# Optimization experiments

Hardware: AMD Instinct MI355X
Metric: run time of the kernel (lower is better)

The kernel has to match this reference:

```python
import jax, jax.numpy as jnp
import numpy as np

EMBED = 128
HEADS = 16
N = 10000
E = 160000
NEG_SLOPE = 0.2


def setup_inputs() -> dict:
    key = jax.random.key(0)
    ks = jax.random.split(key, 12)
    s = 0.05
    return {
        "x": jax.random.normal(ks[0], (N, EMBED), jnp.float32),
        "edge_index": jax.random.randint(ks[1], (2, E), 0, N, jnp.int64),
        # gat1: in=EMBED, out=EMBED, heads=16, concat
        "W1": jax.random.normal(ks[2], (EMBED, HEADS * EMBED), jnp.float32) * s,
        "a_src1": jax.random.normal(ks[3], (HEADS, EMBED), jnp.float32) * s,
        "a_dst1": jax.random.normal(ks[4], (HEADS, EMBED), jnp.float32) * s,
        "b1": jnp.zeros((HEADS * EMBED,), jnp.float32),
        # gat2: in=HEADS*EMBED, out=EMBED, heads=1, no concat
        "W2": jax.random.normal(ks[5], (HEADS * EMBED, EMBED), jnp.float32) * s,
        "a_src2": jax.random.normal(ks[6], (1, EMBED), jnp.float32) * s,
        "a_dst2": jax.random.normal(ks[7], (1, EMBED), jnp.float32) * s,
        "b2": jnp.zeros((EMBED,), jnp.float32),
        # classifier
        "Wc": jax.random.normal(ks[8], (EMBED, 1), jnp.float32) * s,
        "bc": jnp.zeros((1,), jnp.float32),
    }


def _gat_layer(x, src, dst, W, a_src, a_dst, b, heads, out_ch, n_nodes):
    # node projection: [N, H, C]
    h = (x @ W).reshape(n_nodes, heads, out_ch)
    # per-node attention logits [N, H]
    al_s = jnp.einsum('nhc,hc->nh', h, a_src)
    al_d = jnp.einsum('nhc,hc->nh', h, a_dst)
    # per-edge logits [E, H]
    e = jax.nn.leaky_relu(al_s[src] + al_d[dst], NEG_SLOPE)
    # segment softmax over incoming edges of each dst node
    m = jax.ops.segment_max(e, dst, num_segments=n_nodes)
    ex = jnp.exp(e - m[dst])
    z = jax.ops.segment_sum(ex, dst, num_segments=n_nodes)
    alpha = ex / (z[dst] + 1e-16)
    # weighted scatter-aggregate [N, H, C]
    msg = h[src] * alpha[:, :, None]
    out = jax.ops.segment_sum(msg, dst, num_segments=n_nodes)
    return out.reshape(n_nodes, heads * out_ch) + b


def reference(x, edge_index, W1, a_src1, a_dst1, b1, W2, a_src2, a_dst2, b2, Wc, bc):
    n_nodes = x.shape[0]
    # PyG GATConv default: add self loops
    loop = jnp.arange(n_nodes, dtype=edge_index.dtype)
    src = jnp.concatenate([edge_index[0], loop])
    dst = jnp.concatenate([edge_index[1], loop])
    h = _gat_layer(x, src, dst, W1, a_src1, a_dst1, b1, HEADS, EMBED, n_nodes)
    h = jax.nn.elu(h)
    h = _gat_layer(h, src, dst, W2, a_src2, a_dst2, b2, 1, EMBED, n_nodes)
    return h @ Wc + bc  # [N, 1]
```

## Files before the change

### kernel.cpp

```cpp
#include <hip/hip_runtime.h>
#include <hip/hip_bf16.h>

#define EMBED 128
#define HEADS 16
#define NEG 0.2f

typedef __attribute__((ext_vector_type(8))) short short8;
typedef __attribute__((ext_vector_type(4))) float floatx4;

static __device__ __forceinline__ float leaky(float x) { return x > 0.f ? x : NEG * x; }

static __device__ __forceinline__ short f2bf_bits(float f) {
  __hip_bfloat16 h = __float2bfloat16(f);
  union { __hip_bfloat16 b; short s; } u;
  u.b = h;
  return u.s;
}


__global__ void k_hist(const int* __restrict__ ei, int E, int N, int* __restrict__ deg) {
  int i = blockIdx.x * blockDim.x + threadIdx.x;
  int Et = E + N;
  if (i >= Et) return;
  int d = (i < E) ? ei[E + i] : (i - E);
  atomicAdd(&deg[d], 1);
}

__global__ __launch_bounds__(1024) void k_scan(const int* __restrict__ deg,
                                               int* __restrict__ row_ptr,
                                               int* __restrict__ cursor, int N) {
  __shared__ int wsum[16];
  int tid = threadIdx.x;
  int lane = tid & 63, w = tid >> 6;
  int base = 0;
  for (int c0 = 0; c0 < N; c0 += 1024) {
    int i = c0 + tid;
    int v = (i < N) ? deg[i] : 0;
    int s = v;
#pragma unroll
    for (int dd = 1; dd < 64; dd <<= 1) {
      int t = __shfl_up(s, dd);
      if (lane >= dd) s += t;
    }
    if (lane == 63) wsum[w] = s;
    __syncthreads();
    int carry = 0, ctot = 0;
#pragma unroll
    for (int k = 0; k < 16; ++k) {
      int t = wsum[k];
      ctot += t;
      if (k < w) carry += t;
    }
    int excl = base + carry + s - v;
    if (i < N) {
      row_ptr[i] = excl;
      cursor[i] = excl;
    }
    base += ctot;
    __syncthreads();
  }
  if (tid == 0) row_ptr[N] = base;
}

__global__ void k_scatter(const int* __restrict__ ei, int E, int N,
                          int* __restrict__ cursor, int* __restrict__ csr_src) {
  int i = blockIdx.x * blockDim.x + threadIdx.x;
  int Et = E + N;
  if (i >= Et) return;
  int s = (i < E) ? ei[i] : (i - E);
  int d = (i < E) ? ei[E + i] : (i - E);
  int pos = atomicAdd(&cursor[d], 1);
  csr_src[pos] = s;
}


__global__ __launch_bounds__(256) void k_prep(const float* __restrict__ W1,
                                              const float* __restrict__ a_src1,
                                              const float* __restrict__ a_dst1,
                                              const float* __restrict__ W2,
                                              const float* __restrict__ a_src2,
                                              const float* __restrict__ a_dst2,
                                              const float* __restrict__ Wc,
                                              const float* __restrict__ b2,
                                              const float* __restrict__ bc,
                                              float* __restrict__ wsAll,
                                              float* __restrict__ uvec,
                                              float* __restrict__ cconst,
                                              short* __restrict__ hi,
                                              short* __restrict__ lo,
                                              float* __restrict__ part,
                                              int* __restrict__ deg,
                                              int N) {
  __shared__ float tile[64][65];
  if (blockIdx.x < 64) {
    int b = blockIdx.x;
    int h = b & 15;
    int c0 = ((b >> 4) & 1) * 64;
    int j0 = ((b >> 5) & 1) * 64;
    int t = threadIdx.x;
#pragma unroll
    for (int i = 0; i < 4; ++i) {
      int idx4 = i * 256 + t;
      int c = idx4 >> 4, j4 = idx4 & 15;
      float4 v = *(const float4*)&W1[(size_t)(c0 + c) * 2048 + h * 128 + j0 + j4 * 4];
      tile[c][j4 * 4 + 0] = v.x;
      tile[c][j4 * 4 + 1] = v.y;
      tile[c][j4 * 4 + 2] = v.z;
      tile[c][j4 * 4 + 3] = v.w;
    }
    __syncthreads();
#pragma unroll
    for (int i = 0; i < 4; ++i) {
      int idx = i * 256 + t;
      int j = idx >> 4, c4 = idx & 15;
      unsigned short vh[4], vl[4];
#pragma unroll
      for (int ii = 0; ii < 4; ++ii) {
        float wv = tile[c4 * 4 + ii][j];
        short hb = f2bf_bits(wv);
        float hf = __uint_as_float(((unsigned int)(unsigned short)hb) << 16);
        vh[ii] = (unsigned short)hb;
        vl[ii] = (unsigned short)f2bf_bits(wv - hf);
      }
      size_t o = (size_t)h * 16384 + (size_t)(j0 + j) * 128 + c0 + c4 * 4;
      *(ushort4*)&hi[o] = make_ushort4(vh[0], vh[1], vh[2], vh[3]);
      *(ushort4*)&lo[o] = make_ushort4(vl[0], vl[1], vl[2], vl[3]);
    }
    return;
  }
  int gid = (blockIdx.x - 64) * 256 + threadIdx.x;
  if (gid < 4096) {
    int sel = gid >> 11;
    int id = gid & 2047;
    int h = id >> 7, k = id & 127;
    const float* av = sel ? a_dst1 : a_src1;
    float sum = 0.f;
    const float* wrow = W1 + (size_t)k * 2048 + h * 128;
    const float* arow = av + h * 128;
#pragma unroll 4
    for (int c = 0; c < 128; ++c) sum += wrow[c] * arow[c];
    wsAll[gid] = sum;
  } else if (gid < 10240) {
    int g = gid - 4096;
    int sel = g >> 11;
    int k = g & 2047;
    const float* v = sel == 0 ? Wc : (sel == 1 ? a_src2 : a_dst2);
    const float* wrow = W2 + (size_t)k * 128;
    float s = 0.f;
#pragma unroll 4
    for (int j = 0; j < 128; ++j) s += wrow[j] * v[j];
    uvec[g] = s;
  } else if (gid == 10240) {
    float s = 0.f;
    for (int j = 0; j < 128; ++j) s += b2[j] * Wc[j];
    *cconst = s + bc[0];
  } else if (gid >= 10496) {
    int z = gid - 10496;
    if (z < 3 * N) part[z] = 0.f;
    else if (z < 4 * N) deg[z - 3 * N] = 0;
  }
}


__global__ __launch_bounds__(256) void k_al1v2(const float* __restrict__ x,
                                               const float* __restrict__ wsAll,
                                               float* __restrict__ als,
                                               float* __restrict__ ald, int N) {
  __shared__ float wss[128][16], wsd[128][16];
  int tid = threadIdx.x;
  for (int i = tid; i < 2048; i += 256) {
    int h = i >> 7, c = i & 127;
    wss[c][h] = wsAll[i];
    wsd[c][h] = wsAll[2048 + i];
  }
  __syncthreads();
  int gid = blockIdx.x * 256 + tid;
  int n = gid >> 4, h = gid & 15;
  if (n >= N) return;
  const float4* xp = (const float4*)(x + (size_t)n * 128);
  float ps = 0.f, pd = 0.f;
#pragma unroll 8
  for (int c4 = 0; c4 < 32; ++c4) {
    float4 xv = xp[c4];
    int c = c4 * 4;
    ps += xv.x * wss[c][h] + xv.y * wss[c + 1][h] + xv.z * wss[c + 2][h] + xv.w * wss[c + 3][h];
    pd += xv.x * wsd[c][h] + xv.y * wsd[c + 1][h] + xv.z * wsd[c + 2][h] + xv.w * wsd[c + 3][h];
  }
  als[gid] = ps;
  ald[gid] = pd;
}


__global__ __launch_bounds__(256) void k_attn1h(const float* __restrict__ x,
                                                const float* __restrict__ als,
                                                const float* __restrict__ ald,
                                                const int* __restrict__ row_ptr,
                                                const int* __restrict__ csr,
                                                __hip_bfloat16* __restrict__ xaggb,
                                                int N) {
  __shared__ float accsh[2][64][37];

  int tid = threadIdx.x;
  int w = tid >> 6, lane = tid & 63;
  int slot = w >> 1, half = w & 1;
  int d = blockIdx.x * 2 + slot;
  bool active = d < N;

  int e0 = 0, deg = 0;
  if (active) {
    e0 = row_ptr[d];
    deg = row_ptr[d + 1] - e0;
  }

  int g = lane >> 4, c8 = lane & 15;
  float4 aldh4 = make_float4(0.f, 0.f, 0.f, 0.f);
  if (active) aldh4 = *(const float4*)&ald[(size_t)d * 16 + g * 4];

  float acc[4][8];
  float zacc[4] = {0.f, 0.f, 0.f, 0.f};
#pragma unroll
  for (int hh = 0; hh < 4; ++hh)
#pragma unroll
    for (int i = 0; i < 8; ++i) acc[hh][i] = 0.f;

  if (active) {
    int sreg = 0;
    if (lane < deg) sreg = csr[e0 + lane];
    const float* xc = x + c8 * 8;

    int e = half;
    bool have = e < deg;
    int sC = 0;
    float4 alC = make_float4(0.f, 0.f, 0.f, 0.f);
    float4 xaC = alC, xbC = alC;
    if (have) {
      sC = (e < 64) ? __shfl(sreg, e) : csr[e0 + e];
      alC = *(const float4*)&als[(size_t)sC * 16 + g * 4];
      const float4* xp = (const float4*)(xc + (size_t)sC * 128);
      xaC = xp[0];
      xbC = xp[1];
    }
    while (have) {
      int e2 = e + 2;
      bool have2 = e2 < deg;
      int sN = 0;
      float4 alN = alC, xaN = xaC, xbN = xbC;
      if (have2) {
        sN = (e2 < 64) ? __shfl(sreg, e2) : csr[e0 + e2];
        alN = *(const float4*)&als[(size_t)sN * 16 + g * 4];
        const float4* xp2 = (const float4*)(xc + (size_t)sN * 128);
        xaN = xp2[0];
        xbN = xp2[1];
      }
      float ev0 = __expf(leaky(alC.x + aldh4.x));
      float ev1 = __expf(leaky(alC.y + aldh4.y));
      float ev2 = __expf(leaky(alC.z + aldh4.z));
      float ev3 = __expf(leaky(alC.w + aldh4.w));
      zacc[0] += ev0; zacc[1] += ev1; zacc[2] += ev2; zacc[3] += ev3;
      acc[0][0] += ev0 * xaC.x; acc[0][1] += ev0 * xaC.y; acc[0][2] += ev0 * xaC.z; acc[0][3] += ev0 * xaC.w;
      acc[0][4] += ev0 * xbC.x; acc[0][5] += ev0 * xbC.y; acc[0][6] += ev0 * xbC.z; acc[0][7] += ev0 * xbC.w;
      acc[1][0] += ev1 * xaC.x; acc[1][1] += ev1 * xaC.y; acc[1][2] += ev1 * xaC.z; acc[1][3] += ev1 * xaC.w;
      acc[1][4] += ev1 * xbC.x; acc[1][5] += ev1 * xbC.y; acc[1][6] += ev1 * xbC.z; acc[1][7] += ev1 * xbC.w;
      acc[2][0] += ev2 * xaC.x; acc[2][1] += ev2 * xaC.y; acc[2][2] += ev2 * xaC.z; acc[2][3] += ev2 * xaC.w;
      acc[2][4] += ev2 * xbC.x; acc[2][5] += ev2 * xbC.y; acc[2][6] += ev2 * xbC.z; acc[2][7] += ev2 * xbC.w;
      acc[3][0] += ev3 * xaC.x; acc[3][1] += ev3 * xaC.y; acc[3][2] += ev3 * xaC.z; acc[3][3] += ev3 * xaC.w;
      acc[3][4] += ev3 * xbC.x; acc[3][5] += ev3 * xbC.y; acc[3][6] += ev3 * xbC.z; acc[3][7] += ev3 * xbC.w;
      e = e2;
      have = have2;
      sC = sN;
      alC = alN;
      xaC = xaN;
      xbC = xbN;
    }
  }

  if (half == 1) {
#pragma unroll
    for (int hh = 0; hh < 4; ++hh) {
#pragma unroll
      for (int i = 0; i < 8; ++i)
        accsh[slot][lane][hh * 8 + i] = acc[hh][i];
      accsh[slot][lane][32 + hh] = zacc[hh];
    }
  }
  __syncthreads();
  if (half == 0 && active) {
#pragma unroll
    for (int hh = 0; hh < 4; ++hh) {
      int h = g * 4 + hh;
      float z = zacc[hh] + accsh[slot][lane][32 + hh];
      float iz = 1.f / (z + 1e-16f);
      __hip_bfloat16 t[8];
#pragma unroll
      for (int i = 0; i < 8; ++i) {
        float v = (acc[hh][i] + accsh[slot][lane][hh * 8 + i]) * iz;
        t[i] = __float2bfloat16(v);
      }
      *(uint4*)(xaggb + (size_t)h * N * 128 + (size_t)d * 128 + c8 * 8) = *(uint4*)t;
    }
  }
}


__global__ __launch_bounds__(256, 2) void k_fused(const __hip_bfloat16* __restrict__ xaggb,
                                                  const short* __restrict__ w1t_hi,
                                                  const short* __restrict__ w1t_lo,
                                                  const float* __restrict__ b1,
                                                  const float* __restrict__ uvec,
                                                  float* __restrict__ partc,
                                                  float* __restrict__ parts,
                                                  float* __restrict__ partd,
                                                  int N) {
  __shared__ float sh[512];
  __shared__ __align__(16) char Bh[32768];
  __shared__ __align__(16) char Bl[32768];
  int tid = threadIdx.x;
  int h = blockIdx.y;
  int n0 = blockIdx.x * 256;

  for (int i = tid; i < 512; i += 256) {
    int arr = i >> 7, jj = i & 127;
    sh[i] = (arr == 0) ? b1[h * 128 + jj] : uvec[(arr - 1) * 2048 + h * 128 + jj];
  }
  const char* gbh = (const char*)(w1t_hi + (size_t)h * 16384);
  const char* gbl = (const char*)(w1t_lo + (size_t)h * 16384);
#pragma unroll
  for (int i = 0; i < 8; ++i) {
    int ci = i * 256 + tid;
    int row = ci >> 4, kc = ci & 15;
    int po = row * 256 + ((kc ^ (row & 15)) << 4);
    *(uint4*)(Bh + po) = *(const uint4*)(gbh + ci * 16);
    *(uint4*)(Bl + po) = *(const uint4*)(gbl + ci * 16);
  }

  int w = tid >> 6, lane = tid & 63;
  int quad = lane >> 4, l15 = lane & 15;
  int nw = n0 + w * 64;

  const char* abase = (const char*)xaggb + (size_t)h * N * 256;
  short8 a[4][4];
#pragma unroll
  for (int nt = 0; nt < 4; ++nt) {
    int node = nw + nt * 16 + l15;
    if (node >= N) node = N - 1;
    const char* rowp = abase + (size_t)node * 256 + quad * 16;
#pragma unroll
    for (int ks = 0; ks < 4; ++ks)
      a[nt][ks] = *(const short8*)(rowp + ks * 64);
  }
  __syncthreads();

  floatx4 acc[4][8];
#pragma unroll
  for (int jt = 0; jt < 8; ++jt) {
    floatx4 bb = *(const floatx4*)&sh[jt * 16 + quad * 4];
#pragma unroll
    for (int nt = 0; nt < 4; ++nt) acc[nt][jt] = bb;
  }

  for (int ks = 0; ks < 4; ++ks) {
    int xo = (((ks * 4 + quad) ^ l15) << 4);
#pragma unroll
    for (int jt = 0; jt < 8; ++jt) {
      int po = (jt * 16 + l15) * 256 + xo;
      short8 wh = *(const short8*)(Bh + po);
      short8 wl = *(const short8*)(Bl + po);
#pragma unroll
      for (int nt = 0; nt < 4; ++nt) {
        acc[nt][jt] = __builtin_amdgcn_mfma_f32_16x16x32_bf16(wh, a[nt][ks], acc[nt][jt], 0, 0, 0);
        acc[nt][jt] = __builtin_amdgcn_mfma_f32_16x16x32_bf16(wl, a[nt][ks], acc[nt][jt], 0, 0, 0);
      }
    }
  }

  float pc[4] = {0.f, 0.f, 0.f, 0.f};
  float ps[4] = {0.f, 0.f, 0.f, 0.f};
  float pd[4] = {0.f, 0.f, 0.f, 0.f};
#pragma unroll
  for (int jt = 0; jt < 8; ++jt) {
    floatx4 uc = *(const floatx4*)&sh[128 + jt * 16 + quad * 4];
    floatx4 us = *(const floatx4*)&sh[256 + jt * 16 + quad * 4];
    floatx4 ud = *(const floatx4*)&sh[384 + jt * 16 + quad * 4];
#pragma unroll
    for (int nt = 0; nt < 4; ++nt) {
#pragma unroll
      for (int r = 0; r < 4; ++r) {
        float v = acc[nt][jt][r];
        float e = v > 0.f ? v : (__expf(v) - 1.f);
        pc[nt] += e * uc[r];
        ps[nt] += e * us[r];
        pd[nt] += e * ud[r];
      }
    }
  }
#pragma unroll
  for (int nt = 0; nt < 4; ++nt) {
    float c = pc[nt], s = ps[nt], dd = pd[nt];
    c += __shfl_xor(c, 16); c += __shfl_xor(c, 32);
    s += __shfl_xor(s, 16); s += __shfl_xor(s, 32);
    dd += __shfl_xor(dd, 16); dd += __shfl_xor(dd, 32);
    int node = nw + nt * 16 + l15;
    if (quad == 0 && node < N) {
      atomicAdd(&partc[node], c);
      atomicAdd(&parts[node], s);
      atomicAdd(&partd[node], dd);
    }
  }
}


__global__ __launch_bounds__(256) void k_attn2s(const float* __restrict__ partc,
                                                const float* __restrict__ parts,
                                                const float* __restrict__ partd,
                                                const int* __restrict__ row_ptr,
                                                const int* __restrict__ csr,
                                                const float* __restrict__ cconst,
                                                float* __restrict__ out, int N) {
  int grp = threadIdx.x >> 4, l = threadIdx.x & 15;
  int d = blockIdx.x * 16 + grp;
  if (d >= N) return;
  int e0 = row_ptr[d], deg = row_ptr[d + 1] - e0;
  float aldd = partd[d];
  float z = 0.f, num = 0.f;
  for (int e = l; e < deg; e += 16) {
    int s = csr[e0 + e];
    float v = __expf(leaky(parts[s] + aldd));
    z += v;
    num += v * partc[s];
  }
#pragma unroll
  for (int off = 8; off; off >>= 1) {
    z += __shfl_xor(z, off);
    num += __shfl_xor(num, off);
  }
  if (l == 0) out[d] = num / (z + 1e-16f) + cconst[0];
}


extern "C" void kernel_launch(void* const* d_in, const int* in_sizes, int n_in,
                              void* d_out, int out_size, void* d_ws, size_t ws_size,
                              hipStream_t stream) {
  const float* x      = (const float*)d_in[0];
  const int*   ei     = (const int*)d_in[1];
  const float* W1     = (const float*)d_in[2];
  const float* a_src1 = (const float*)d_in[3];
  const float* a_dst1 = (const float*)d_in[4];
  const float* b1     = (const float*)d_in[5];
  const float* W2     = (const float*)d_in[6];
  const float* a_src2 = (const float*)d_in[7];
  const float* a_dst2 = (const float*)d_in[8];
  const float* b2     = (const float*)d_in[9];
  const float* Wc     = (const float*)d_in[10];
  const float* bc     = (const float*)d_in[11];

  int N = in_sizes[0] / EMBED;
  int E = in_sizes[1] / 2;
  int Et = E + N;

  char* ws = (char*)d_ws;
  size_t off = 0;
  auto alloc = [&](size_t bytes) -> void* {
    void* p = ws + off;
    off += (bytes + 255) & ~(size_t)255;
    return p;
  };
  __hip_bfloat16* xaggb = (__hip_bfloat16*)alloc((size_t)N * 2048 * 2 + 65536);
  short* w1t_hi = (short*)alloc((size_t)262144 * 2);
  short* w1t_lo = (short*)alloc((size_t)262144 * 2);
  float* wsAll  = (float*)alloc(4096 * 4);
  float* uvec   = (float*)alloc(6144 * 4);
  float* cconst = (float*)alloc(256);
  float* als1   = (float*)alloc((size_t)N * 16 * 4);
  float* ald1   = (float*)alloc((size_t)N * 16 * 4);
  float* part   = (float*)alloc((size_t)3 * N * 4);
  float* partc  = part;
  float* parts  = part + N;
  float* partd  = part + 2 * N;
  int* deg      = (int*)alloc((size_t)N * 4);
  int* row_ptr  = (int*)alloc((size_t)(N + 1) * 4);
  int* cursor   = (int*)alloc((size_t)N * 4);
  int* csr      = (int*)alloc((size_t)Et * 4);

  int nPrepB = 64 + (10496 + 4 * N + 255) / 256;
  k_prep<<<nPrepB, 256, 0, stream>>>(W1, a_src1, a_dst1, W2, a_src2, a_dst2, Wc, b2, bc,
                                     wsAll, uvec, cconst, w1t_hi, w1t_lo, part, deg, N);
  k_hist<<<(Et + 255) / 256, 256, 0, stream>>>(ei, E, N, deg);
  k_scan<<<1, 1024, 0, stream>>>(deg, row_ptr, cursor, N);
  k_scatter<<<(Et + 255) / 256, 256, 0, stream>>>(ei, E, N, cursor, csr);
  k_al1v2<<<(N * 16 + 255) / 256, 256, 0, stream>>>(x, wsAll, als1, ald1, N);
  k_attn1h<<<(N + 1) / 2, 256, 0, stream>>>(x, als1, ald1, row_ptr, csr, xaggb, N);
  k_fused<<<dim3((N + 255) / 256, 16), 256, 0, stream>>>(xaggb, w1t_hi, w1t_lo, b1, uvec,
                                                         partc, parts, partd, N);
  k_attn2s<<<(N + 15) / 16, 256, 0, stream>>>(partc, parts, partd, row_ptr, csr, cconst,
                                              (float*)d_out, N);
}
```

Measured before the change: 183.5 us.

## Merge scatter with layer-1 logits kernel, use direct-to-LDS loads, interleave partials

Folds the CSR scatter kernel and the per-node layer-1 attention logit kernel into one launch, with the block index choosing the role. This saves a kernel launch and lets the two independent jobs overlap. In the fused MFMA kernel, the swizzled W1 tile now goes from global memory straight into LDS through global_load_lds instead of passing through registers, and the MFMA loop runs at raised wave priority via s_setprio. The source-logit and classifier partials are packed into one float2 array, so each edge in the layer-2 softmax needs one 8-byte gather instead of two 4-byte gathers. The catch is that the merged kernel reserves LDS even for the scatter blocks, and the direct-LDS path relies on the swizzle being applied on the source side instead of the destination.

```diff
diff --git a/kernel.cpp b/kernel.cpp
--- a/kernel.cpp
+++ b/kernel.cpp
@@ -7,6 +7,11 @@
 
 typedef __attribute__((ext_vector_type(8))) short short8;
 typedef __attribute__((ext_vector_type(4))) float floatx4;
+
+#define GLOAD_LDS16(g, l)                                                                  \
+  __builtin_amdgcn_global_load_lds((const __attribute__((address_space(1))) unsigned int*)(g), \
+                                   (__attribute__((address_space(3))) unsigned int*)(l),       \
+                                   16, 0, 0)
 
 static __device__ __forceinline__ float leaky(float x) { return x > 0.f ? x : NEG * x; }
 
@@ -62,15 +67,46 @@
   if (tid == 0) row_ptr[N] = base;
 }
 
-__global__ void k_scatter(const int* __restrict__ ei, int E, int N,
-                          int* __restrict__ cursor, int* __restrict__ csr_src) {
-  int i = blockIdx.x * blockDim.x + threadIdx.x;
-  int Et = E + N;
-  if (i >= Et) return;
-  int s = (i < E) ? ei[i] : (i - E);
-  int d = (i < E) ? ei[E + i] : (i - E);
-  int pos = atomicAdd(&cursor[d], 1);
-  csr_src[pos] = s;
+
+__global__ __launch_bounds__(256) void k_scat_al1(const int* __restrict__ ei, int E, int N,
+                                                  int* __restrict__ cursor,
+                                                  int* __restrict__ csr_src,
+                                                  const float* __restrict__ x,
+                                                  const float* __restrict__ wsAll,
+                                                  float* __restrict__ als,
+                                                  float* __restrict__ ald, int nScat) {
+  __shared__ float wss[128][16], wsd[128][16];
+  if ((int)blockIdx.x < nScat) {
+    int i = blockIdx.x * 256 + threadIdx.x;
+    int Et = E + N;
+    if (i >= Et) return;
+    int s = (i < E) ? ei[i] : (i - E);
+    int d = (i < E) ? ei[E + i] : (i - E);
+    int pos = atomicAdd(&cursor[d], 1);
+    csr_src[pos] = s;
+    return;
+  }
+  int tid = threadIdx.x;
+  for (int i = tid; i < 2048; i += 256) {
+    int h = i >> 7, c = i & 127;
+    wss[c][h] = wsAll[i];
+    wsd[c][h] = wsAll[2048 + i];
+  }
+  __syncthreads();
+  int gid = ((int)blockIdx.x - nScat) * 256 + tid;
+  int n = gid >> 4, h = gid & 15;
+  if (n >= N) return;
+  const float4* xp = (const float4*)(x + (size_t)n * 128);
+  float ps = 0.f, pd = 0.f;
+#pragma unroll 8
+  for (int c4 = 0; c4 < 32; ++c4) {
+    float4 xv = xp[c4];
+    int c = c4 * 4;
+    ps += xv.x * wss[c][h] + xv.y * wss[c + 1][h] + xv.z * wss[c + 2][h] + xv.w * wss[c + 3][h];
+    pd += xv.x * wsd[c][h] + xv.y * wsd[c + 1][h] + xv.z * wsd[c + 2][h] + xv.w * wsd[c + 3][h];
+  }
+  als[gid] = ps;
+  ald[gid] = pd;
 }
 
 
@@ -159,35 +195,6 @@
     if (z < 3 * N) part[z] = 0.f;
     else if (z < 4 * N) deg[z - 3 * N] = 0;
   }
-}
-
-
-__global__ __launch_bounds__(256) void k_al1v2(const float* __restrict__ x,
-                                               const float* __restrict__ wsAll,
-                                               float* __restrict__ als,
-                                               float* __restrict__ ald, int N) {
-  __shared__ float wss[128][16], wsd[128][16];
-  int tid = threadIdx.x;
-  for (int i = tid; i < 2048; i += 256) {
-    int h = i >> 7, c = i & 127;
-    wss[c][h] = wsAll[i];
-    wsd[c][h] = wsAll[2048 + i];
-  }
-  __syncthreads();
-  int gid = blockIdx.x * 256 + tid;
-  int n = gid >> 4, h = gid & 15;
-  if (n >= N) return;
-  const float4* xp = (const float4*)(x + (size_t)n * 128);
-  float ps = 0.f, pd = 0.f;
-#pragma unroll 8
-  for (int c4 = 0; c4 < 32; ++c4) {
-    float4 xv = xp[c4];
-    int c = c4 * 4;
-    ps += xv.x * wss[c][h] + xv.y * wss[c + 1][h] + xv.z * wss[c + 2][h] + xv.w * wss[c + 3][h];
-    pd += xv.x * wsd[c][h] + xv.y * wsd[c + 1][h] + xv.z * wsd[c + 2][h] + xv.w * wsd[c + 3][h];
-  }
-  als[gid] = ps;
-  ald[gid] = pd;
 }
 
 
@@ -307,8 +314,7 @@
                                                   const short* __restrict__ w1t_lo,
                                                   const float* __restrict__ b1,
                                                   const float* __restrict__ uvec,
-                                                  float* __restrict__ partc,
-                                                  float* __restrict__ parts,
+                                                  float2* __restrict__ part2,
                                                   float* __restrict__ partd,
                                                   int N) {
   __shared__ float sh[512];
@@ -318,19 +324,20 @@
   int h = blockIdx.y;
   int n0 = blockIdx.x * 256;
 
+  const char* gbh = (const char*)(w1t_hi + (size_t)h * 16384);
+  const char* gbl = (const char*)(w1t_lo + (size_t)h * 16384);
+#pragma unroll
+  for (int i = 0; i < 8; ++i) {
+    int ci = i * 256 + tid;
+    int row4 = (ci >> 4) & 15;
+    int srcoff = ((ci & ~15) | ((ci & 15) ^ row4)) << 4;
+    GLOAD_LDS16(gbh + srcoff, Bh + ci * 16);
+    GLOAD_LDS16(gbl + srcoff, Bl + ci * 16);
+  }
+
   for (int i = tid; i < 512; i += 256) {
     int arr = i >> 7, jj = i & 127;
     sh[i] = (arr == 0) ? b1[h * 128 + jj] : uvec[(arr - 1) * 2048 + h * 128 + jj];
-  }
-  const char* gbh = (const char*)(w1t_hi + (size_t)h * 16384);
-  const char* gbl = (const char*)(w1t_lo + (size_t)h * 16384);
-#pragma unroll
-  for (int i = 0; i < 8; ++i) {
-    int ci = i * 256 + tid;
-    int row = ci >> 4, kc = ci & 15;
-    int po = row * 256 + ((kc ^ (row & 15)) << 4);
-    *(uint4*)(Bh + po) = *(const uint4*)(gbh + ci * 16);
-    *(uint4*)(Bl + po) = *(const uint4*)(gbl + ci * 16);
   }
 
   int w = tid >> 6, lane = tid & 63;
@@ -358,6 +365,7 @@
     for (int nt = 0; nt < 4; ++nt) acc[nt][jt] = bb;
   }
 
+  __builtin_amdgcn_s_setprio(1);
   for (int ks = 0; ks < 4; ++ks) {
     int xo = (((ks * 4 + quad) ^ l15) << 4);
 #pragma unroll
@@ -372,6 +380,7 @@
       }
     }
   }
+  __builtin_amdgcn_s_setprio(0);
 
   float pc[4] = {0.f, 0.f, 0.f, 0.f};
   float ps[4] = {0.f, 0.f, 0.f, 0.f};
@@ -401,16 +410,15 @@
     dd += __shfl_xor(dd, 16); dd += __shfl_xor(dd, 32);
     int node = nw + nt * 16 + l15;
     if (quad == 0 && node < N) {
-      atomicAdd(&partc[node], c);
-      atomicAdd(&parts[node], s);
+      atomicAdd(&part2[node].x, s);
+      atomicAdd(&part2[node].y, c);
       atomicAdd(&partd[node], dd);
     }
   }
 }
 
 
-__global__ __launch_bounds__(256) void k_attn2s(const float* __restrict__ partc,
-                                                const float* __restrict__ parts,
+__global__ __launch_bounds__(256) void k_attn2s(const float2* __restrict__ part2,
                                                 const float* __restrict__ partd,
                                                 const int* __restrict__ row_ptr,
                                                 const int* __restrict__ csr,
@@ -424,9 +432,10 @@
   float z = 0.f, num = 0.f;
   for (int e = l; e < deg; e += 16) {
     int s = csr[e0 + e];
-    float v = __expf(leaky(parts[s] + aldd));
+    float2 v2 = part2[s];
+    float v = __expf(leaky(v2.x + aldd));
     z += v;
-    num += v * partc[s];
+    num += v * v2.y;
   }
 #pragma unroll
   for (int off = 8; off; off >>= 1) {
@@ -473,24 +482,26 @@
   float* als1   = (float*)alloc((size_t)N * 16 * 4);
   float* ald1   = (float*)alloc((size_t)N * 16 * 4);
   float* part   = (float*)alloc((size_t)3 * N * 4);
-  float* partc  = part;
-  float* parts  = part + N;
+  float2* part2 = (float2*)part;
   float* partd  = part + 2 * N;
   int* deg      = (int*)alloc((size_t)N * 4);
   int* row_ptr  = (int*)alloc((size_t)(N + 1) * 4);
   int* cursor   = (int*)alloc((size_t)N * 4);
   int* csr      = (int*)alloc((size_t)Et * 4);
 
+  int nScat = (Et + 255) / 256;
+  int nAl1  = (N * 16 + 255) / 256;
+
   int nPrepB = 64 + (10496 + 4 * N + 255) / 256;
   k_prep<<<nPrepB, 256, 0, stream>>>(W1, a_src1, a_dst1, W2, a_src2, a_dst2, Wc, b2, bc,
                                      wsAll, uvec, cconst, w1t_hi, w1t_lo, part, deg, N);
   k_hist<<<(Et + 255) / 256, 256, 0, stream>>>(ei, E, N, deg);
   k_scan<<<1, 1024, 0, stream>>>(deg, row_ptr, cursor, N);
-  k_scatter<<<(Et + 255) / 256, 256, 0, stream>>>(ei, E, N, cursor, csr);
-  k_al1v2<<<(N * 16 + 255) / 256, 256, 0, stream>>>(x, wsAll, als1, ald1, N);
+  k_scat_al1<<<nScat + nAl1, 256, 0, stream>>>(ei, E, N, cursor, csr, x, wsAll, als1, ald1,
+                                               nScat);
   k_attn1h<<<(N + 1) / 2, 256, 0, stream>>>(x, als1, ald1, row_ptr, csr, xaggb, N);
   k_fused<<<dim3((N + 255) / 256, 16), 256, 0, stream>>>(xaggb, w1t_hi, w1t_lo, b1, uvec,
-                                                         partc, parts, partd, N);
-  k_attn2s<<<(N + 15) / 16, 256, 0, stream>>>(partc, parts, partd, row_ptr, csr, cconst,
+                                                         part2, partd, N);
+  k_attn2s<<<(N + 15) / 16, 256, 0, stream>>>(part2, partd, row_ptr, csr, cconst,
                                               (float*)d_out, N);
 }
```

Result: faster. 179.5 us (-2.2%).
